# Optimization experiments

Measured on AMD Instinct MI355X. Metric: run time of the kernel, lower is better.

## Reference

```python
import jax, jax.numpy as jnp
import numpy as np

B, H, W, C = 16, 32, 32, 512
NUM_HEADS = 8
ATTN_DIM = 512
HEAD_DIM = ATTN_DIM // NUM_HEADS
EPS = 1e-5


def setup_inputs() -> dict:
    key = jax.random.key(0)
    ks = jax.random.split(key, 6)
    s_in = 1.0 / np.sqrt(C)
    s_attn = 1.0 / np.sqrt(ATTN_DIM)
    return {
        "x": jax.random.normal(ks[0], (B, H, W, C), dtype=jnp.float32),
        "gamma": jnp.ones((C,), dtype=jnp.float32),
        "beta": jnp.zeros((C,), dtype=jnp.float32),
        "wq": jax.random.normal(ks[1], (C, ATTN_DIM), dtype=jnp.float32) * s_in,
        "bq": jnp.zeros((ATTN_DIM,), dtype=jnp.float32),
        "wk": jax.random.normal(ks[2], (C, ATTN_DIM), dtype=jnp.float32) * s_in,
        "bk": jnp.zeros((ATTN_DIM,), dtype=jnp.float32),
        "wv": jax.random.normal(ks[3], (C, ATTN_DIM), dtype=jnp.float32) * s_in,
        "bv": jnp.zeros((ATTN_DIM,), dtype=jnp.float32),
        "wo": jax.random.normal(ks[4], (ATTN_DIM, C), dtype=jnp.float32) * s_attn,
        "bo": jnp.zeros((C,), dtype=jnp.float32),
    }


def reference(x, gamma, beta, wq, bq, wk, bk, wv, bv, wo, bo):
    b, h, w, c = x.shape
    t = h * w  # number of spatial tokens
    # GroupNorm with 1 group: normalize over (H, W, C) per sample
    mean = jnp.mean(x, axis=(1, 2, 3), keepdims=True)
    var = jnp.var(x, axis=(1, 2, 3), keepdims=True)
    xn = (x - mean) * jax.lax.rsqrt(var + EPS) * gamma + beta
    xn = xn.reshape(b, t, c)
    # 1x1-conv q/k/v == dense over channel dim; split into heads
    q = (xn @ wq + bq).reshape(b, t, NUM_HEADS, HEAD_DIM)
    k = (xn @ wk + bk).reshape(b, t, NUM_HEADS, HEAD_DIM)
    v = (xn @ wv + bv).reshape(b, t, NUM_HEADS, HEAD_DIM)
    scale = 1.0 / jnp.sqrt(jnp.asarray(HEAD_DIM, dtype=x.dtype))
    scores = jnp.einsum('bqhd,bkhd->bhqk', q, k) * scale
    probs = jax.nn.softmax(scores, axis=-1)
    attn = jnp.einsum('bhqk,bkhd->bqhd', probs, v).reshape(b, t, ATTN_DIM)
    out = attn @ wo + bo
    # Multiplex([None, branch]): residual add, then Reshape([-1, model_dim])
    return x.reshape(b, t, c) + out
```

## Files before the change

### kernel.cpp

```cpp
#include <hip/hip_runtime.h>
#include <hip/hip_bf16.h>

typedef __attribute__((ext_vector_type(8))) short short8;
typedef __attribute__((ext_vector_type(4))) short short4v;
typedef __attribute__((ext_vector_type(4))) float f32x4;

#define B_ 16
#define T_ 1024
#define C_ 512
#define NH 8
#define HD 64

__device__ __forceinline__ short f2bf(float f) {
  union { float f; unsigned u; } v;
  v.f = f;
  unsigned r = v.u + 0x7fffu + ((v.u >> 16) & 1u);
  return (short)(r >> 16);
}

__device__ __forceinline__ short2 pack_bf2(float a, float b) {
  __hip_bfloat162 t = __float22bfloat162_rn(make_float2(a, b));
  short2 r;
  __builtin_memcpy(&r, &t, 4);
  return r;
}

__device__ __forceinline__ float fexp2(float x) {
  float r;
  asm("v_exp_f32 %0, %1" : "=v"(r) : "v"(x));
  return r;
}

__device__ __forceinline__ void gload_lds16(const short* g, short* l) {
  __builtin_amdgcn_global_load_lds(
      (const __attribute__((address_space(1))) void*)g,
      (__attribute__((address_space(3))) void*)l, 16, 0, 0);
}

__global__ __launch_bounds__(256) void stats1_kernel(const float* __restrict__ x,
                                                     float2* __restrict__ partials) {
  int chunk = blockIdx.x;
  int b = blockIdx.y;
  int tid = threadIdx.x;
  const float4* xb = (const float4*)(x + (size_t)b * 524288 + (size_t)chunk * 8192);
  float s = 0.f, s2 = 0.f;
#pragma unroll
  for (int i = 0; i < 8; i++) {
    float4 v = xb[tid + i * 256];
    s  += v.x + v.y + v.z + v.w;
    s2 += v.x * v.x + v.y * v.y + v.z * v.z + v.w * v.w;
  }
  __shared__ float ls[256], ls2[256];
  ls[tid] = s; ls2[tid] = s2;
  __syncthreads();
  for (int o = 128; o > 0; o >>= 1) {
    if (tid < o) { ls[tid] += ls[tid + o]; ls2[tid] += ls2[tid + o]; }
    __syncthreads();
  }
  if (tid == 0) partials[b * 64 + chunk] = make_float2(ls[0], ls2[0]);
}

__global__ __launch_bounds__(64) void stats2_kernel(const float2* __restrict__ partials,
                                                    float* __restrict__ stats) {
  int b = blockIdx.x;
  float2 p = partials[b * 64 + threadIdx.x];
  float s = p.x, s2 = p.y;
#pragma unroll
  for (int off = 1; off < 64; off <<= 1) {
    s  += __shfl_xor(s,  off, 64);
    s2 += __shfl_xor(s2, off, 64);
  }
  if (threadIdx.x == 0) {
    float mean = s * (1.f / 524288.f);
    float var  = s2 * (1.f / 524288.f) - mean * mean;
    stats[b * 2]     = mean;
    stats[b * 2 + 1] = rsqrtf(var + 1e-5f);
  }
}

__global__ __launch_bounds__(256) void norm_kernel(const float* __restrict__ x,
                                                   const float* __restrict__ gamma,
                                                   const float* __restrict__ beta,
                                                   const float* __restrict__ stats,
                                                   short* __restrict__ xn) {
  size_t i4 = (size_t)blockIdx.x * 256 + threadIdx.x;
  float4 v = ((const float4*)x)[i4];
  size_t i = i4 * 4;
  int b = (int)(i >> 19);
  int c = (int)(i & 511);
  float mean = stats[b * 2], rstd = stats[b * 2 + 1];
  short4v o;
  o[0] = f2bf((v.x - mean) * rstd * gamma[c + 0] + beta[c + 0]);
  o[1] = f2bf((v.y - mean) * rstd * gamma[c + 1] + beta[c + 1]);
  o[2] = f2bf((v.z - mean) * rstd * gamma[c + 2] + beta[c + 2]);
  o[3] = f2bf((v.w - mean) * rstd * gamma[c + 3] + beta[c + 3]);
  ((short4v*)xn)[i4] = o;
}

__global__ __launch_bounds__(256) void transpose_w_all(const float* __restrict__ wq,
                                                       const float* __restrict__ wk,
                                                       const float* __restrict__ wv,
                                                       const float* __restrict__ wo,
                                                       short* __restrict__ wqkvT,
                                                       short* __restrict__ woT) {
  int o = blockIdx.x * 256 + threadIdx.x;
  int sel = o >> 18;
  int oo = o & 262143;
  int k = oo >> 9, n = oo & 511;
  const float* w = (sel == 0) ? wq : (sel == 1) ? wk : (sel == 2) ? wv : wo;
  float val = w[oo];
  if (sel < 3) wqkvT[((size_t)(sel * 512 + n)) * 512 + k] = f2bf(val);
  else         woT[(size_t)n * 512 + k] = f2bf(val);
}

__global__ __launch_bounds__(256) void gemm_qkv(const short* __restrict__ A,
                                                const short* __restrict__ Bt,
                                                const float* __restrict__ bq,
                                                const float* __restrict__ bk,
                                                const float* __restrict__ bv,
                                                short* __restrict__ C) {
  __shared__ __align__(16) short As[128 * 32];
  __shared__ __align__(16) short Bs[128 * 32];
  int tid = threadIdx.x;
  int w = tid >> 6, lane = tid & 63;
  int quad = lane >> 4, l16 = lane & 15;
  int mw = (w >> 1) * 64, nw = (w & 1) * 64;
  int seg = (blockIdx.x * 128) >> 9;
  const float* bias = (seg == 0) ? bq : (seg == 1) ? bk : bv;
  float smul = (seg == 0) ? 0.18033688011112042f : 1.0f;
  const short* Atile = A + (size_t)(blockIdx.y * 128) * 512;
  const short* Btile = Bt + (size_t)(blockIdx.x * 128) * 512;
  int srow = (w << 4) + (lane >> 2);
  int scol = (lane & 3) * 8;
  f32x4 acc[4][4] = {};
  for (int k0 = 0; k0 < 512; k0 += 32) {
    __syncthreads();
    gload_lds16(&Atile[(size_t)srow * 512 + k0 + scol],        &As[w * 512]);
    gload_lds16(&Atile[(size_t)(srow + 64) * 512 + k0 + scol], &As[2048 + w * 512]);
    gload_lds16(&Btile[(size_t)srow * 512 + k0 + scol],        &Bs[w * 512]);
    gload_lds16(&Btile[(size_t)(srow + 64) * 512 + k0 + scol], &Bs[2048 + w * 512]);
    __syncthreads();
    short8 af[4], bf[4];
#pragma unroll
    for (int i = 0; i < 4; i++) af[i] = *(const short8*)(&As[(mw + i * 16 + l16) * 32 + quad * 8]);
#pragma unroll
    for (int i = 0; i < 4; i++) bf[i] = *(const short8*)(&Bs[(nw + i * 16 + l16) * 32 + quad * 8]);
#pragma unroll
    for (int mi = 0; mi < 4; mi++)
#pragma unroll
      for (int ni = 0; ni < 4; ni++)
        acc[mi][ni] = __builtin_amdgcn_mfma_f32_16x16x32_bf16(af[mi], bf[ni], acc[mi][ni], 0, 0, 0);
  }
  int m0 = blockIdx.y * 128 + mw;
  int n0 = blockIdx.x * 128 + nw;
#pragma unroll
  for (int mi = 0; mi < 4; mi++)
#pragma unroll
    for (int ni = 0; ni < 4; ni++) {
      int col = n0 + ni * 16 + l16;
      float bval = bias[col & 511];
#pragma unroll
      for (int r = 0; r < 4; r++) {
        int row = m0 + mi * 16 + quad * 4 + r;
        C[(size_t)row * 1536 + col] = f2bf((acc[mi][ni][r] + bval) * smul);
      }
    }
}

__global__ __launch_bounds__(256) void gemm_out(const short* __restrict__ A,
                                                const short* __restrict__ Bt,
                                                const float* __restrict__ bias,
                                                const float* __restrict__ xres,
                                                float* __restrict__ out) {
  __shared__ __align__(16) short As[128 * 32];
  __shared__ __align__(16) short Bs[128 * 32];
  int tid = threadIdx.x;
  int w = tid >> 6, lane = tid & 63;
  int quad = lane >> 4, l16 = lane & 15;
  int mw = (w >> 1) * 64, nw = (w & 1) * 64;
  const short* Atile = A + (size_t)(blockIdx.y * 128) * 512;
  const short* Btile = Bt + (size_t)(blockIdx.x * 128) * 512;
  int srow = (w << 4) + (lane >> 2);
  int scol = (lane & 3) * 8;
  f32x4 acc[4][4] = {};
  for (int k0 = 0; k0 < 512; k0 += 32) {
    __syncthreads();
    gload_lds16(&Atile[(size_t)srow * 512 + k0 + scol],        &As[w * 512]);
    gload_lds16(&Atile[(size_t)(srow + 64) * 512 + k0 + scol], &As[2048 + w * 512]);
    gload_lds16(&Btile[(size_t)srow * 512 + k0 + scol],        &Bs[w * 512]);
    gload_lds16(&Btile[(size_t)(srow + 64) * 512 + k0 + scol], &Bs[2048 + w * 512]);
    __syncthreads();
    short8 af[4], bf[4];
#pragma unroll
    for (int i = 0; i < 4; i++) af[i] = *(const short8*)(&As[(mw + i * 16 + l16) * 32 + quad * 8]);
#pragma unroll
    for (int i = 0; i < 4; i++) bf[i] = *(const short8*)(&Bs[(nw + i * 16 + l16) * 32 + quad * 8]);
#pragma unroll
    for (int mi = 0; mi < 4; mi++)
#pragma unroll
      for (int ni = 0; ni < 4; ni++)
        acc[mi][ni] = __builtin_amdgcn_mfma_f32_16x16x32_bf16(af[mi], bf[ni], acc[mi][ni], 0, 0, 0);
  }
  int m0 = blockIdx.y * 128 + mw;
  int n0 = blockIdx.x * 128 + nw;
#pragma unroll
  for (int mi = 0; mi < 4; mi++)
#pragma unroll
    for (int ni = 0; ni < 4; ni++) {
      int col = n0 + ni * 16 + l16;
      float bval = bias[col];
#pragma unroll
      for (int r = 0; r < 4; r++) {
        int row = m0 + mi * 16 + quad * 4 + r;
        out[(size_t)row * 512 + col] = acc[mi][ni][r] + bval + xres[(size_t)row * 512 + col];
      }
    }
}

__global__ __launch_bounds__(256) void vtrans_kernel(const short* __restrict__ qkv,
                                                     short* __restrict__ vT) {
  int chunk = blockIdx.x;
  int h  = blockIdx.y;
  int b  = blockIdx.z;
  int tid = threadIdx.x;
  __shared__ short TB[128 * 72];
  const short* src = qkv + ((size_t)b * T_ + chunk * 128) * 1536 + 1024 + (size_t)h * 64;
#pragma unroll
  for (int i = 0; i < 4; i++) {
    int idx = tid + i * 256;
    int t = idx >> 3, c = idx & 7;
    *(short8*)(&TB[t * 72 + c * 8]) = *(const short8*)(src + (size_t)t * 1536 + c * 8);
  }
  __syncthreads();
  short* dst = vT + ((size_t)(b * 8 + h) * 64) * 1024 + chunk * 128;
#pragma unroll
  for (int i = 0; i < 4; i++) {
    int idx = tid + i * 256;
    int d = idx >> 4, sc = idx & 15;
    int w2 = sc >> 2, q2 = sc & 3;
    short8 o;
#pragma unroll
    for (int sg = 0; sg < 8; sg++) {
      int half = sg >> 2, r = sg & 3;
      o[sg] = TB[(half * 64 + w2 * 16 + q2 * 4 + r) * 72 + d];
    }
    *(short8*)(dst + (size_t)d * 1024 + sc * 8) = o;
  }
}

__global__ __launch_bounds__(256) void attn_kernel(const short* __restrict__ Q,
                                                   const short* __restrict__ Kmat,
                                                   const short* __restrict__ vTg,
                                                   short* __restrict__ O) {
  int tid = threadIdx.x;
  int w = tid >> 6, lane = tid & 63;
  int quad = lane >> 4, l16 = lane & 15;
  int bh = blockIdx.x;
  int qt = blockIdx.y;
  int b = bh >> 3, h = bh & 7;
  size_t base  = ((size_t)b * T_) * 1536 + (size_t)h * 64;
  size_t vbase = ((size_t)bh * 64) * 1024;
  size_t obase = ((size_t)b * T_) * 512 + (size_t)h * 64;
  int qrow0 = qt * 64;

  __shared__ __align__(16) char smem[17408 + 1024];
  float* Lbuf = (float*)smem;
  float* denomL = (float*)(smem + 17408);

  short8 qf0[4], qf1[4];
#pragma unroll
  for (int g = 0; g < 4; g++) {
    const short* qp = Q + base + (size_t)(qrow0 + g * 16 + l16) * 1536 + quad * 8;
    qf0[g] = *(const short8*)qp;
    qf1[g] = *(const short8*)(qp + 32);
  }

  const short* kp0 = Kmat + base + (size_t)(w * 16 + l16) * 1536 + quad * 8;
  const short* kp1 = kp0 + 64 * 1536;
  const short* vp0 = vTg + vbase + (size_t)l16 * 1024 + (w * 4 + quad) * 8;

  f32x4 oacc[4][4] = {};
  float lsum[4] = {0.f, 0.f, 0.f, 0.f};

  short8 ka0 = *(const short8*)kp0;
  short8 ka1 = *(const short8*)(kp0 + 32);
  short8 ka2 = *(const short8*)kp1;
  short8 ka3 = *(const short8*)(kp1 + 32);

#pragma unroll
  for (int t = 0; t < 8; t++) {
    short8 vfr[4];
#pragma unroll
    for (int f = 0; f < 4; f++)
      vfr[f] = *(const short8*)(vp0 + (size_t)f * 16384 + t * 128);
    short8 kn0, kn1, kn2, kn3;
    if (t < 7) {
      const short* p0 = kp0 + (size_t)(t + 1) * 196608;
      const short* p1 = kp1 + (size_t)(t + 1) * 196608;
      kn0 = *(const short8*)p0;
      kn1 = *(const short8*)(p0 + 32);
      kn2 = *(const short8*)p1;
      kn3 = *(const short8*)(p1 + 32);
    }
#pragma unroll
    for (int g = 0; g < 4; g++) {
      f32x4 za = {}, zb = {};
      za = __builtin_amdgcn_mfma_f32_16x16x32_bf16(ka0, qf0[g], za, 0, 0, 0);
      za = __builtin_amdgcn_mfma_f32_16x16x32_bf16(ka1, qf1[g], za, 0, 0, 0);
      zb = __builtin_amdgcn_mfma_f32_16x16x32_bf16(ka2, qf0[g], zb, 0, 0, 0);
      zb = __builtin_amdgcn_mfma_f32_16x16x32_bf16(ka3, qf1[g], zb, 0, 0, 0);
      float pa0 = fexp2(za[0]), pa1 = fexp2(za[1]);
      float pa2 = fexp2(za[2]), pa3 = fexp2(za[3]);
      float pb0 = fexp2(zb[0]), pb1 = fexp2(zb[1]);
      float pb2 = fexp2(zb[2]), pb3 = fexp2(zb[3]);
      lsum[g] += (pa0 + pa1) + (pa2 + pa3) + ((pb0 + pb1) + (pb2 + pb3));
      short2 a01 = pack_bf2(pa0, pa1), a23 = pack_bf2(pa2, pa3);
      short2 b01 = pack_bf2(pb0, pb1), b23 = pack_bf2(pb2, pb3);
      short8 pf;
      pf[0] = a01.x; pf[1] = a01.y; pf[2] = a23.x; pf[3] = a23.y;
      pf[4] = b01.x; pf[5] = b01.y; pf[6] = b23.x; pf[7] = b23.y;
#pragma unroll
      for (int f = 0; f < 4; f++)
        oacc[f][g] = __builtin_amdgcn_mfma_f32_16x16x32_bf16(vfr[f], pf, oacc[f][g], 0, 0, 0);
    }
    if (t < 7) { ka0 = kn0; ka1 = kn1; ka2 = kn2; ka3 = kn3; }
  }

#pragma unroll
  for (int g = 0; g < 4; g++) {
    lsum[g] += __shfl_xor(lsum[g], 16, 64);
    lsum[g] += __shfl_xor(lsum[g], 32, 64);
  }
  if (quad == 0) {
#pragma unroll
    for (int g = 0; g < 4; g++) denomL[w * 64 + g * 16 + l16] = lsum[g];
  }
  for (int ww = 0; ww < 4; ww++) {
    __syncthreads();
    if (w == ww) {
#pragma unroll
      for (int g = 0; g < 4; g++)
#pragma unroll
        for (int f = 0; f < 4; f++) {
          float* p = &Lbuf[(g * 16 + l16) * 68 + f * 16 + quad * 4];
          if (ww == 0) *(f32x4*)p = oacc[f][g];
          else         *(f32x4*)p = *(f32x4*)p + oacc[f][g];
        }
    }
  }
  __syncthreads();

  int q = tid >> 2, seg = tid & 3;
  float dn = denomL[q] + denomL[64 + q] + denomL[128 + q] + denomL[192 + q];
  float rinv = __frcp_rn(dn);
  const float* row = &Lbuf[q * 68 + seg * 16];
  short8 o0, o1;
#pragma unroll
  for (int i = 0; i < 8; i++) o0[i] = f2bf(row[i] * rinv);
#pragma unroll
  for (int i = 0; i < 8; i++) o1[i] = f2bf(row[8 + i] * rinv);
  short* op = O + obase + (size_t)(qrow0 + q) * 512 + seg * 16;
  *(short8*)op = o0;
  *(short8*)(op + 8) = o1;
}

extern "C" void kernel_launch(void* const* d_in, const int* in_sizes, int n_in,
                              void* d_out, int out_size, void* d_ws, size_t ws_size,
                              hipStream_t stream) {
  const float* x     = (const float*)d_in[0];
  const float* gamma = (const float*)d_in[1];
  const float* beta  = (const float*)d_in[2];
  const float* wq    = (const float*)d_in[3];
  const float* bq    = (const float*)d_in[4];
  const float* wk    = (const float*)d_in[5];
  const float* bk    = (const float*)d_in[6];
  const float* wv    = (const float*)d_in[7];
  const float* bv    = (const float*)d_in[8];
  const float* wo    = (const float*)d_in[9];
  const float* bo    = (const float*)d_in[10];
  float* out = (float*)d_out;

  char* ws = (char*)d_ws;
  const size_t XN_ELEMS = (size_t)B_ * T_ * C_;
  size_t off = 0;
  float* stats = (float*)(ws + off); off += 256;
  float2* partials = (float2*)(ws + off); off += 16 * 64 * sizeof(float2);
  short* xn    = (short*)(ws + off); off += XN_ELEMS * 2;
  short* wqkvT = (short*)(ws + off); off += (size_t)1536 * 512 * 2;
  short* woT   = (short*)(ws + off); off += (size_t)512 * 512 * 2;
  short* qkv   = (short*)(ws + off); off += (size_t)B_ * T_ * 1536 * 2;
  short* vTb   = (short*)(ws + off); off += XN_ELEMS * 2;
  short* ao    = (short*)(ws + off); off += XN_ELEMS * 2;

  stats1_kernel<<<dim3(64, 16), 256, 0, stream>>>(x, partials);
  stats2_kernel<<<16, 64, 0, stream>>>(partials, stats);
  norm_kernel<<<8192, 256, 0, stream>>>(x, gamma, beta, stats, xn);
  transpose_w_all<<<4096, 256, 0, stream>>>(wq, wk, wv, wo, wqkvT, woT);

  gemm_qkv<<<dim3(12, 128), 256, 0, stream>>>(xn, wqkvT, bq, bk, bv, qkv);

  vtrans_kernel<<<dim3(8, 8, 16), 256, 0, stream>>>(qkv, vTb);
  attn_kernel<<<dim3(128, 16), 256, 0, stream>>>(qkv, qkv + 512, vTb, ao);

  gemm_out<<<dim3(4, 128), 256, 0, stream>>>(ao, woT, bo, x, out);
}
```

Baseline: 254.1 us.

## Stage K tiles through double-buffered swizzled LDS via direct global-to-LDS loads

K fragments were previously loaded straight from global memory into registers with a strided per-lane pattern. They are now brought into a double-buffered LDS area with coalesced direct global-to-LDS loads and an XOR swizzle, and read back as MFMA fragments from LDS. The aim is more coalesced K traffic and prefetch of the next tile without holding it in registers. The cost is a __syncthreads per iteration and roughly double the shared memory, which may lower occupancy. The loop relies on gload_lds16 completing before the barrier, with no explicit vmcnt wait visible, so correctness depends on that helper.

```diff
diff --git a/kernel.cpp b/kernel.cpp
--- a/kernel.cpp
+++ b/kernel.cpp
@@ -263,9 +263,12 @@
   size_t obase = ((size_t)b * T_) * 512 + (size_t)h * 64;
   int qrow0 = qt * 64;
 
-  __shared__ __align__(16) char smem[17408 + 1024];
+  __shared__ __align__(16) char smem[32768 + 1024];
+  short* KTb[2];
+  KTb[0] = (short*)smem;
+  KTb[1] = (short*)(smem + 16384);
   float* Lbuf = (float*)smem;
-  float* denomL = (float*)(smem + 17408);
+  float* denomL = (float*)(smem + 32768);
 
   short8 qf0[4], qf1[4];
 #pragma unroll
@@ -275,40 +278,56 @@
     qf1[g] = *(const short8*)(qp + 32);
   }
 
-  const short* kp0 = Kmat + base + (size_t)(w * 16 + l16) * 1536 + quad * 8;
-  const short* kp1 = kp0 + 64 * 1536;
+  const short* ksrc[4];
+#pragma unroll
+  for (int n = 0; n < 4; n++) {
+    int bk = w * 256 + n * 64 + lane;
+    int key = bk >> 3, jc = bk & 7;
+    int dcol = jc ^ (key & 7);
+    ksrc[n] = Kmat + base + (size_t)key * 1536 + dcol * 8;
+  }
+
   const short* vp0 = vTg + vbase + (size_t)l16 * 1024 + (w * 4 + quad) * 8;
+
+  int l7 = l16 & 7;
+  int kA0 = ((w * 16 + l16) * 8 + (quad ^ l7)) * 8;
+  int kA1 = ((w * 16 + l16) * 8 + ((quad + 4) ^ l7)) * 8;
+  int kB0 = kA0 + 4096;
+  int kB1 = kA1 + 4096;
 
   f32x4 oacc[4][4] = {};
   float lsum[4] = {0.f, 0.f, 0.f, 0.f};
 
-  short8 ka0 = *(const short8*)kp0;
-  short8 ka1 = *(const short8*)(kp0 + 32);
-  short8 ka2 = *(const short8*)kp1;
-  short8 ka3 = *(const short8*)(kp1 + 32);
+#pragma unroll
+  for (int n = 0; n < 4; n++)
+    gload_lds16(ksrc[n], KTb[0] + (w * 256 + n * 64) * 8);
 
 #pragma unroll
   for (int t = 0; t < 8; t++) {
+    short* KTc = KTb[t & 1];
+    short* KTn = KTb[(t + 1) & 1];
+    __syncthreads();
     short8 vfr[4];
 #pragma unroll
     for (int f = 0; f < 4; f++)
       vfr[f] = *(const short8*)(vp0 + (size_t)f * 16384 + t * 128);
-    short8 kn0, kn1, kn2, kn3;
     if (t < 7) {
-      const short* p0 = kp0 + (size_t)(t + 1) * 196608;
-      const short* p1 = kp1 + (size_t)(t + 1) * 196608;
-      kn0 = *(const short8*)p0;
-      kn1 = *(const short8*)(p0 + 32);
-      kn2 = *(const short8*)p1;
-      kn3 = *(const short8*)(p1 + 32);
-    }
+#pragma unroll
+      for (int n = 0; n < 4; n++)
+        gload_lds16(ksrc[n] + (size_t)(t + 1) * 196608, KTn + (w * 256 + n * 64) * 8);
+    }
+    short8 ka0 = *(const short8*)(KTc + kA0);
+    short8 ka1 = *(const short8*)(KTc + kA1);
+    short8 kb0 = *(const short8*)(KTc + kB0);
+    short8 kb1 = *(const short8*)(KTc + kB1);
+
 #pragma unroll
     for (int g = 0; g < 4; g++) {
       f32x4 za = {}, zb = {};
       za = __builtin_amdgcn_mfma_f32_16x16x32_bf16(ka0, qf0[g], za, 0, 0, 0);
       za = __builtin_amdgcn_mfma_f32_16x16x32_bf16(ka1, qf1[g], za, 0, 0, 0);
-      zb = __builtin_amdgcn_mfma_f32_16x16x32_bf16(ka2, qf0[g], zb, 0, 0, 0);
-      zb = __builtin_amdgcn_mfma_f32_16x16x32_bf16(ka3, qf1[g], zb, 0, 0, 0);
+      zb = __builtin_amdgcn_mfma_f32_16x16x32_bf16(kb0, qf0[g], zb, 0, 0, 0);
+      zb = __builtin_amdgcn_mfma_f32_16x16x32_bf16(kb1, qf1[g], zb, 0, 0, 0);
       float pa0 = fexp2(za[0]), pa1 = fexp2(za[1]);
       float pa2 = fexp2(za[2]), pa3 = fexp2(za[3]);
       float pb0 = fexp2(zb[0]), pb1 = fexp2(zb[1]);
@@ -323,7 +342,6 @@
       for (int f = 0; f < 4; f++)
         oacc[f][g] = __builtin_amdgcn_mfma_f32_16x16x32_bf16(vfr[f], pf, oacc[f][g], 0, 0, 0);
     }
-    if (t < 7) { ka0 = kn0; ka1 = kn1; ka2 = kn2; ka3 = kn3; }
   }
 
 #pragma unroll
```

Measured after the change: 252.7 us. No clear change (-0.5%).
